# Kernel tuning notes

Measured on AMD Instinct MI355X. Metric: run time of the kernel, lower is better.

The kernel has to match this reference:

```python
import jax, jax.numpy as jnp
import numpy as np

H_SIZE = 1024
N_HEADS = 16
HEAD_DIM = H_SIZE // N_HEADS
TAU2 = 1.0
LN_EPS = 1e-5


def setup_inputs() -> dict:
    key = jax.random.key(0)
    ks = jax.random.split(key, 12)
    B, S = 2, 1024
    s = 1.0 / np.sqrt(H_SIZE)
    inp = {
        "input": jax.random.normal(ks[0], (B, S, H_SIZE), dtype=jnp.float32),
        "input_mask": jnp.ones((B, S), dtype=jnp.float32),
        # uniform(0,1) noise; converted to Gumbel(0,1) inside reference
        "gumbel": jax.random.uniform(ks[1], (B, N_HEADS, S, S), dtype=jnp.float32,
                                     minval=1e-10, maxval=1.0),
        "Wq": jax.random.normal(ks[2], (H_SIZE, H_SIZE), dtype=jnp.float32) * s,
        "bq": jnp.zeros((H_SIZE,), dtype=jnp.float32),
        "Wk": jax.random.normal(ks[3], (H_SIZE, H_SIZE), dtype=jnp.float32) * s,
        "bk": jnp.zeros((H_SIZE,), dtype=jnp.float32),
        "Wv": jax.random.normal(ks[4], (H_SIZE, H_SIZE), dtype=jnp.float32) * s,
        "bv": jnp.zeros((H_SIZE,), dtype=jnp.float32),
        "Wo": jax.random.normal(ks[5], (H_SIZE, H_SIZE), dtype=jnp.float32) * s,
        "bo": jnp.zeros((H_SIZE,), dtype=jnp.float32),
        "gamma": jnp.ones((H_SIZE,), dtype=jnp.float32),
        "beta": jnp.zeros((H_SIZE,), dtype=jnp.float32),
    }
    return inp


def reference(input, input_mask, gumbel, Wq, bq, Wk, bk, Wv, bv, Wo, bo, gamma, beta):
    B, S, _ = input.shape
    # projections -> [B, H, S, D]
    def proj(W, b):
        y = jnp.einsum('bsh,oh->bso', input, W) + b  # torch Linear: x @ W.T + b
        return y.reshape(B, S, N_HEADS, HEAD_DIM).transpose(0, 2, 1, 3)
    qq = proj(Wq, bq)
    kk = proj(Wk, bk)
    vv = proj(Wv, bv)
    # raw scores (NOTE: original has no 1/sqrt(d) scaling)
    interact = jnp.einsum('bhqd,bhkd->bhqk', qq, kk)
    # gumbel-softmax (soft): softmax((logits + g)/tau)
    g = -jnp.log(-jnp.log(gumbel))
    sto_attn = jax.nn.softmax((interact + g) / TAU2, axis=-1)
    # masking: mask_1 over query dim, mask_2 over key dim
    mask = input_mask[:, None, :, None] * input_mask[:, None, None, :]  # [B,1,S,S]
    attn = sto_attn * mask
    # (dropout p=0 -> identity)
    out = jnp.einsum('bhqk,bhkd->bhqd', attn, vv)
    out = out.transpose(0, 2, 1, 3).reshape(B, S, H_SIZE)
    out = jnp.einsum('bsh,oh->bso', out, Wo) + bo
    # residual + layernorm
    x = out + input
    mu = jnp.mean(x, axis=-1, keepdims=True)
    var = jnp.mean(jnp.square(x - mu), axis=-1, keepdims=True)
    return (x - mu) * jax.lax.rsqrt(var + LN_EPS) * gamma + beta
```

## Files before the change

kernel.cpp:

```cpp
#include <hip/hip_runtime.h>

#define S_LEN 1024
#define HSZ   1024
#define NHEAD 16
#define HD    64
#define BATCH 2
#define MROWS 2048
#define SOFTMAX_M0 50.0f

typedef unsigned short u16;
typedef __attribute__((ext_vector_type(8))) short short8;
typedef __attribute__((ext_vector_type(4))) short short4v;
typedef __attribute__((ext_vector_type(4))) float f32x4;

#define MFMA_BF16(a, b, c) __builtin_amdgcn_mfma_f32_16x16x32_bf16((a), (b), (c), 0, 0, 0)

__device__ __forceinline__ u16 f2bf(float f) {
    union { float f; unsigned u; } c; c.f = f;
    unsigned u = c.u;
    u += 0x7fffu + ((u >> 16) & 1u);
    return (u16)(u >> 16);
}
__device__ __forceinline__ float bf2f(u16 s) {
    union { unsigned u; float f; } c; c.u = ((unsigned)s) << 16;
    return c.f;
}
__device__ __forceinline__ short8 ld8(const u16* p) {
    return *reinterpret_cast<const short8*>(p);
}
__device__ __forceinline__ void gld16(const u16* g, u16* l) {
    __builtin_amdgcn_global_load_lds(
        (const __attribute__((address_space(1))) unsigned int*)g,
        (__attribute__((address_space(3))) unsigned int*)l, 16, 0, 0);
}
__device__ __forceinline__ f32x4 ld4_nt(const float* p) {
    return __builtin_nontemporal_load(reinterpret_cast<const f32x4*>(p));
}
__device__ __forceinline__ int frag_off(int row, int cbb) {
    return (((row << 3) | (cbb ^ (row & 7))) << 3);
}

template<int MT>
__device__ __forceinline__ void gemm_tile(const u16* __restrict__ Ag,
                                          const u16* __restrict__ Bg,
                                          int klen, u16* As, u16* Bs,
                                          f32x4 (&acc)[MT][4]) {
    const int tid  = threadIdx.x;
    const int wave = tid >> 6, lane = tid & 63;
    const int lr = lane & 15, grp = lane >> 4;
    const int wm = wave >> 1, wn = wave & 1;
    const int ASZ = MT * 2048;
    const int BSZ = 8192;

#pragma unroll
    for (int mt = 0; mt < MT; mt++)
#pragma unroll
        for (int nt = 0; nt < 4; nt++)
            acc[mt][nt] = (f32x4){0.f, 0.f, 0.f, 0.f};

    auto stage = [&](int k0, u16* Ah, u16* Bh) {
#pragma unroll
        for (int j = 0; j < MT; j++) {
            int c = j * 256 + tid, row = c >> 3, cb = (c & 7) ^ (row & 7);
            gld16(Ag + (size_t)row * HSZ + k0 + cb * 8, Ah + c * 8);
        }
#pragma unroll
        for (int j = 0; j < 4; j++) {
            int c = j * 256 + tid, row = c >> 3, cb = (c & 7) ^ (row & 7);
            gld16(Bg + (size_t)row * HSZ + k0 + cb * 8, Bh + c * 8);
        }
    };

    stage(0, As, Bs);

    for (int k0 = 0; k0 < klen; k0 += 64) {
        const int cur = (k0 >> 6) & 1;
        const u16* Ac = As + cur * ASZ;
        const u16* Bc = Bs + cur * BSZ;
        __syncthreads();
        if (k0 + 64 < klen)
            stage(k0 + 64, As + (cur ^ 1) * ASZ, Bs + (cur ^ 1) * BSZ);

#pragma unroll
        for (int h = 0; h < 2; h++) {
            const int cbb = h * 4 + grp;
            short8 af[MT], bf[4];
#pragma unroll
            for (int mt = 0; mt < MT; mt++)
                af[mt] = ld8(Ac + frag_off(wm * (MT * 16) + mt * 16 + lr, cbb));
#pragma unroll
            for (int nt = 0; nt < 4; nt++)
                bf[nt] = ld8(Bc + frag_off(wn * 64 + nt * 16 + lr, cbb));
#pragma unroll
            for (int mt = 0; mt < MT; mt++)
#pragma unroll
                for (int nt = 0; nt < 4; nt++)
                    acc[mt][nt] = MFMA_BF16(af[mt], bf[nt], acc[mt][nt]);
        }
    }
}

__global__ __launch_bounds__(256)
void convert_kernel(const float* __restrict__ x,  const float* __restrict__ wq,
                    const float* __restrict__ wk, const float* __restrict__ wv,
                    const float* __restrict__ wo, u16* __restrict__ dst) {
    const int XV = (MROWS * HSZ) / 4;
    const int WV = (HSZ * HSZ) / 4;
    int vid = blockIdx.x * 256 + threadIdx.x;
    const float* src; int off;
    if (vid < XV)            { src = x;  off = vid; }
    else if (vid < XV + WV)  { src = wq; off = vid - XV; }
    else if (vid < XV + 2*WV){ src = wk; off = vid - XV - WV; }
    else if (vid < XV + 3*WV){ src = wv; off = vid - XV - 2*WV; }
    else                     { src = wo; off = vid - XV - 3*WV; }
    float4 v = reinterpret_cast<const float4*>(src)[off];
    ushort4 o;
    o.x = f2bf(v.x); o.y = f2bf(v.y); o.z = f2bf(v.z); o.w = f2bf(v.w);
    reinterpret_cast<ushort4*>(dst)[vid] = o;
}

__global__ __launch_bounds__(256)
void qkv_gemm(const u16* __restrict__ xb,
              const u16* __restrict__ wqb, const u16* __restrict__ wkb,
              const u16* __restrict__ wvb,
              const float* __restrict__ bq, const float* __restrict__ bk,
              const float* __restrict__ bv, const float* __restrict__ mask,
              u16* __restrict__ qout, u16* __restrict__ kout,
              u16* __restrict__ vtout) {
    __shared__ u16 As[2 * 64 * 64];
    __shared__ u16 Bs[2 * 128 * 64];
    const int ntile = blockIdx.x;
    const int mtile = blockIdx.y;
    const int p  = ntile >> 3;
    const int m0 = mtile * 64;
    const int nw = (ntile & 7) * 128;
    const u16*  W    = (p == 0) ? wqb : (p == 1) ? wkb : wvb;
    const float* bias = (p == 0) ? bq : (p == 1) ? bk : bv;

    f32x4 acc[2][4];
    gemm_tile<2>(xb + (size_t)m0 * HSZ, W + (size_t)nw * HSZ, HSZ, As, Bs, acc);

    const int wave = threadIdx.x >> 6, lane = threadIdx.x & 63;
    const int lr = lane & 15, grp = lane >> 4;
    const int wm = wave >> 1, wn = wave & 1;
#pragma unroll
    for (int mt = 0; mt < 2; mt++)
#pragma unroll
        for (int nt = 0; nt < 4; nt++)
#pragma unroll
            for (int r = 0; r < 4; r++) {
                int m = m0 + wm * 32 + mt * 16 + grp * 4 + r;
                int o = nw + wn * 64 + nt * 16 + lr;
                float val = acc[mt][nt][r] + bias[o];
                int b = m >> 10, s = m & 1023, hh = o >> 6, d = o & 63;
                if (p == 0)
                    qout[(((size_t)(b * NHEAD + hh)) * S_LEN + s) * HD + d] = f2bf(val);
                else if (p == 1)
                    kout[(((size_t)(b * NHEAD + hh)) * S_LEN + s) * HD + d] = f2bf(val);
                else
                    vtout[(((size_t)(b * NHEAD + hh)) * HD + d) * S_LEN + s] =
                        f2bf(val * mask[m]);
            }
}

__global__ __launch_bounds__(256, 4)
void attn_kernel(const u16* __restrict__ qb, const u16* __restrict__ kb,
                 const u16* __restrict__ vt, const float* __restrict__ gumbel,
                 u16* __restrict__ po, float* __restrict__ pl) {
    const int bh   = blockIdx.y;
    const int qt   = blockIdx.x;
    const int half = blockIdx.z;
    const int q0 = qt * 64, kbase = half * 512;
    const int tid = threadIdx.x;
    const int wave = tid >> 6, lane = tid & 63;
    const int lr = lane & 15, grp = lane >> 4;

    const u16* Q = qb + (size_t)bh * S_LEN * HD;
    const u16* K = kb + (size_t)bh * S_LEN * HD;
    const u16* V = vt + (size_t)bh * HD * S_LEN;
    const int qw = q0 + wave * 16;
    const float* Gp = gumbel + (size_t)bh * S_LEN * S_LEN + (size_t)(qw + lr) * S_LEN;

    __shared__ u16 Ks[2][64 * 64];
    __shared__ u16 Vs[2][64 * 64];
    __shared__ u16 pbuf[4 * 16 * 64];
    u16* pw = pbuf + wave * (16 * 64);

    short8 aq0 = ld8(Q + (size_t)(qw + lr) * HD + grp * 8);
    short8 aq1 = ld8(Q + (size_t)(qw + lr) * HD + 32 + grp * 8);

    f32x4 acco[4];
#pragma unroll
    for (int i = 0; i < 4; i++) acco[i] = (f32x4){0.f, 0.f, 0.f, 0.f};
    float lsum = 0.f;

    f32x4 gc[4], gn[4];
#pragma unroll
    for (int kt = 0; kt < 4; kt++)
        gc[kt] = ld4_nt(Gp + kbase + kt * 16 + grp * 4);

    auto stageKV = [&](int k0, int buf) {
#pragma unroll
        for (int j = 0; j < 2; j++) {
            int c = j * 256 + tid, row = c >> 3, cb = (c & 7) ^ (row & 7);
            gld16(K + (size_t)(k0 + row) * HD + cb * 8, Ks[buf] + c * 8);
        }
#pragma unroll
        for (int j = 0; j < 2; j++) {
            int c = j * 256 + tid, row = c >> 3, cb = (c & 7) ^ (row & 7);
            gld16(V + (size_t)row * S_LEN + k0 + cb * 8, Vs[buf] + c * 8);
        }
    };
    stageKV(kbase, 0);

#pragma unroll 1
    for (int it = 0; it < 8; it++) {
        const int k0 = kbase + it * 64;
        const int cur = it & 1;

        __syncthreads();
        if (it < 7) {
            stageKV(k0 + 64, cur ^ 1);
#pragma unroll
            for (int kt = 0; kt < 4; kt++)
                gn[kt] = ld4_nt(Gp + k0 + 64 + kt * 16 + grp * 4);
        }

#pragma unroll
        for (int kt = 0; kt < 4; kt++) {
            short8 kf0 = ld8(Ks[cur] + frag_off(kt * 16 + lr, grp));
            short8 kf1 = ld8(Ks[cur] + frag_off(kt * 16 + lr, 4 + grp));
            f32x4 a = (f32x4){0.f, 0.f, 0.f, 0.f};
            a = MFMA_BF16(kf0, aq0, a);
            a = MFMA_BF16(kf1, aq1, a);
            float p[4];
#pragma unroll
            for (int r = 0; r < 4; r++) {
                float w = -__builtin_amdgcn_rcpf(__logf(gc[kt][r]));
                p[r] = __expf(a[r] - SOFTMAX_M0) * w;
                lsum += p[r];
            }
            ushort4 pk;
            pk.x = f2bf(p[0]); pk.y = f2bf(p[1]);
            pk.z = f2bf(p[2]); pk.w = f2bf(p[3]);
            *reinterpret_cast<ushort4*>(
                pw + lr * 64 + (((kt * 16 + grp * 4) ^ ((lr & 7) << 3)))) = pk;
        }

        short8 pa[2];
#pragma unroll
        for (int ks = 0; ks < 2; ks++) {
            const u16* pp = pw + lr * 64 + (((ks * 32 + grp * 8) ^ ((lr & 7) << 3)));
            short4v lo = *reinterpret_cast<const short4v*>(pp);
            short4v hi = *reinterpret_cast<const short4v*>(pp + 4);
            pa[ks] = __builtin_shufflevector(lo, hi, 0, 1, 2, 3, 4, 5, 6, 7);
        }

#pragma unroll
        for (int nt = 0; nt < 4; nt++)
#pragma unroll
            for (int ks = 0; ks < 2; ks++)
                acco[nt] = MFMA_BF16(pa[ks],
                                     ld8(Vs[cur] + frag_off(nt * 16 + lr, ks * 4 + grp)),
                                     acco[nt]);

        if (it < 7) {
#pragma unroll
            for (int kt = 0; kt < 4; kt++) gc[kt] = gn[kt];
        }
    }

    lsum += __shfl_xor(lsum, 16, 64);
    lsum += __shfl_xor(lsum, 32, 64);

    const int qbase = ((half * 32 + bh) * 16 + qt) * 64 + wave * 16;
    if (lane < 16) pl[qbase + lane] = lsum;

    const int qidx = qbase + grp * 4;
#pragma unroll
    for (int nt = 0; nt < 4; nt++)
#pragma unroll
        for (int r = 0; r < 4; r++)
            po[(size_t)(qidx + r) * 64 + nt * 16 + lr] = f2bf(acco[nt][r]);
}

__global__ __launch_bounds__(256)
void combine_kernel(const u16* __restrict__ po, const float* __restrict__ pl,
                    const float* __restrict__ mask, u16* __restrict__ ctx) {
    const int qt = blockIdx.x, bh = blockIdx.y;
    const int b = bh >> 4, h = bh & 15;
    const int q = threadIdx.x >> 2;
    const int dc = (threadIdx.x & 3) * 16;
    const int i0 = ((0 * 32 + bh) * 16 + qt) * 64 + q;
    const int i1 = ((1 * 32 + bh) * 16 + qt) * 64 + q;
    float l = pl[i0] + pl[i1];
    float mq = mask[b * S_LEN + qt * 64 + q] / l;
    u16* dst = ctx + ((size_t)(b * S_LEN + qt * 64 + q)) * HSZ + h * 64 + dc;
#pragma unroll
    for (int c = 0; c < 2; c++) {
        short8 a = ld8(po + (size_t)i0 * 64 + dc + c * 8);
        short8 bm = ld8(po + (size_t)i1 * 64 + dc + c * 8);
        short8 o;
#pragma unroll
        for (int j = 0; j < 8; j++)
            o[j] = (short)f2bf((bf2f((u16)a[j]) + bf2f((u16)bm[j])) * mq);
        *reinterpret_cast<short8*>(dst + c * 8) = o;
    }
}

__global__ __launch_bounds__(256)
void oproj_gemm(const u16* __restrict__ A, const u16* __restrict__ W,
                float* __restrict__ part0, float* __restrict__ part1) {
    __shared__ u16 As[2 * 64 * 64];
    __shared__ u16 Bs[2 * 128 * 64];
    const int ntile = blockIdx.x;
    const int mtile = blockIdx.y;
    const int z     = blockIdx.z;
    const int m0 = mtile * 64, n0 = ntile * 128, koff = z * 512;

    f32x4 acc[2][4];
    gemm_tile<2>(A + (size_t)m0 * HSZ + koff, W + (size_t)n0 * HSZ + koff,
                 512, As, Bs, acc);

    float* dst = z ? part1 : part0;
    const int wave = threadIdx.x >> 6, lane = threadIdx.x & 63;
    const int lr = lane & 15, grp = lane >> 4;
    const int wm = wave >> 1, wn = wave & 1;
#pragma unroll
    for (int mt = 0; mt < 2; mt++)
#pragma unroll
        for (int nt = 0; nt < 4; nt++)
#pragma unroll
            for (int r = 0; r < 4; r++) {
                int m = m0 + wm * 32 + mt * 16 + grp * 4 + r;
                int o = n0 + wn * 64 + nt * 16 + lr;
                dst[(size_t)m * HSZ + o] = acc[mt][nt][r];
            }
}

__global__ __launch_bounds__(256)
void ln_kernel(const float* __restrict__ part0, const float* __restrict__ part1,
               const float* __restrict__ xin, const float* __restrict__ bo,
               const float* __restrict__ gamma, const float* __restrict__ beta,
               float* __restrict__ out) {
    const int row = blockIdx.x;
    const int tid = threadIdx.x;
    const size_t base = (size_t)row * (HSZ / 4);

    float4 p0 = reinterpret_cast<const float4*>(part0)[base + tid];
    float4 p1 = reinterpret_cast<const float4*>(part1)[base + tid];
    float4 xr = reinterpret_cast<const float4*>(xin)[base + tid];
    float4 bb = reinterpret_cast<const float4*>(bo)[tid];
    float4 v;
    v.x = p0.x + p1.x + xr.x + bb.x;
    v.y = p0.y + p1.y + xr.y + bb.y;
    v.z = p0.z + p1.z + xr.z + bb.z;
    v.w = p0.w + p1.w + xr.w + bb.w;

    float s  = v.x + v.y + v.z + v.w;
    float ss = v.x * v.x + v.y * v.y + v.z * v.z + v.w * v.w;
#pragma unroll
    for (int off = 1; off < 64; off <<= 1) {
        s  += __shfl_xor(s, off, 64);
        ss += __shfl_xor(ss, off, 64);
    }
    __shared__ float red[8];
    int wave = tid >> 6, lane = tid & 63;
    if (lane == 0) { red[wave] = s; red[4 + wave] = ss; }
    __syncthreads();
    s  = red[0] + red[1] + red[2] + red[3];
    ss = red[4] + red[5] + red[6] + red[7];
    float mu  = s * (1.f / HSZ);
    float var = ss * (1.f / HSZ) - mu * mu;
    float rstd = rsqrtf(var + 1e-5f);

    float4 g  = reinterpret_cast<const float4*>(gamma)[tid];
    float4 be = reinterpret_cast<const float4*>(beta)[tid];
    float4 o;
    o.x = (v.x - mu) * rstd * g.x + be.x;
    o.y = (v.y - mu) * rstd * g.y + be.y;
    o.z = (v.z - mu) * rstd * g.z + be.z;
    o.w = (v.w - mu) * rstd * g.w + be.w;
    reinterpret_cast<float4*>(out)[base + tid] = o;
}

extern "C" void kernel_launch(void* const* d_in, const int* in_sizes, int n_in,
                              void* d_out, int out_size, void* d_ws, size_t ws_size,
                              hipStream_t stream) {
    (void)in_sizes; (void)n_in; (void)out_size; (void)ws_size;
    const float* x     = (const float*)d_in[0];
    const float* mask  = (const float*)d_in[1];
    const float* gum   = (const float*)d_in[2];
    const float* Wq    = (const float*)d_in[3];
    const float* bq    = (const float*)d_in[4];
    const float* Wk    = (const float*)d_in[5];
    const float* bk    = (const float*)d_in[6];
    const float* Wv    = (const float*)d_in[7];
    const float* bv    = (const float*)d_in[8];
    const float* Wo    = (const float*)d_in[9];
    const float* bo    = (const float*)d_in[10];
    const float* gamma = (const float*)d_in[11];
    const float* beta  = (const float*)d_in[12];
    float* out = (float*)d_out;

    u16* xb  = (u16*)d_ws;
    u16* wqb = xb  + 2097152;
    u16* wkb = wqb + 1048576;
    u16* wvb = wkb + 1048576;
    u16* wob = wvb + 1048576;
    u16* qb  = wob + 1048576;
    u16* kb  = qb  + 2097152;
    u16* vt  = kb  + 2097152;
    u16* ctx = vt  + 2097152;
    float* part0 = (float*)(ctx + 2097152);
    float* pl    = (float*)((char*)part0 + 8388608);
    u16*   po    = xb;
    float* part1 = (float*)xb;

    convert_kernel<<<dim3(6144), dim3(256), 0, stream>>>(x, Wq, Wk, Wv, Wo, xb);
    qkv_gemm<<<dim3(24, 32), dim3(256), 0, stream>>>(xb, wqb, wkb, wvb,
                                                     bq, bk, bv, mask,
                                                     qb, kb, vt);
    attn_kernel<<<dim3(16, 32, 2), dim3(256), 0, stream>>>(qb, kb, vt, gum, po, pl);
    combine_kernel<<<dim3(16, 32), dim3(256), 0, stream>>>(po, pl, mask, ctx);
    oproj_gemm<<<dim3(8, 32, 2), dim3(256), 0, stream>>>(ctx, wob, part0, part1);
    ln_kernel<<<dim3(2048), dim3(256), 0, stream>>>(part0, part1, x, bo,
                                                    gamma, beta, out);
}
```

Baseline: 293.1 us.

## Split attention key range into four chunks and drop K/V double buffering

The attention kernel now splits the key dimension into four 256-key chunks instead of two 512-key halves, doubling the grid to 2048 blocks. It drops the double-buffered K/V shared tiles to cut LDS use, and raises the occupancy hint to 6 blocks per CU. Staging becomes synchronous, with two barriers per iteration, and the combine kernel now sums four partials. The partial output buffer moves to a separate workspace region. The aim is more parallelism and latency hiding on the gumbel-bandwidth-bound kernel, at the cost of exposed K/V load latency and extra partial traffic.

Result: slower. 382.2 us (+30.4%).

```diff
diff --git a/kernel.cpp b/kernel.cpp
--- a/kernel.cpp
+++ b/kernel.cpp
@@ -163,14 +163,14 @@
             }
 }
 
-__global__ __launch_bounds__(256, 4)
+__global__ __launch_bounds__(256, 6)
 void attn_kernel(const u16* __restrict__ qb, const u16* __restrict__ kb,
                  const u16* __restrict__ vt, const float* __restrict__ gumbel,
                  u16* __restrict__ po, float* __restrict__ pl) {
-    const int bh   = blockIdx.y;
-    const int qt   = blockIdx.x;
-    const int half = blockIdx.z;
-    const int q0 = qt * 64, kbase = half * 512;
+    const int bh  = blockIdx.y;
+    const int qt  = blockIdx.x;
+    const int qtr = blockIdx.z;
+    const int q0 = qt * 64, kbase = qtr * 256;
     const int tid = threadIdx.x;
     const int wave = tid >> 6, lane = tid & 63;
     const int lr = lane & 15, grp = lane >> 4;
@@ -181,8 +181,8 @@
     const int qw = q0 + wave * 16;
     const float* Gp = gumbel + (size_t)bh * S_LEN * S_LEN + (size_t)(qw + lr) * S_LEN;
 
-    __shared__ u16 Ks[2][64 * 64];
-    __shared__ u16 Vs[2][64 * 64];
+    __shared__ u16 Ks[64 * 64];
+    __shared__ u16 Vs[64 * 64];
     __shared__ u16 pbuf[4 * 16 * 64];
     u16* pw = pbuf + wave * (16 * 64);
 
@@ -199,28 +199,24 @@
     for (int kt = 0; kt < 4; kt++)
         gc[kt] = ld4_nt(Gp + kbase + kt * 16 + grp * 4);
 
-    auto stageKV = [&](int k0, int buf) {
+#pragma unroll 1
+    for (int it = 0; it < 4; it++) {
+        const int k0 = kbase + it * 64;
+
+        __syncthreads();
 #pragma unroll
         for (int j = 0; j < 2; j++) {
             int c = j * 256 + tid, row = c >> 3, cb = (c & 7) ^ (row & 7);
-            gld16(K + (size_t)(k0 + row) * HD + cb * 8, Ks[buf] + c * 8);
+            gld16(K + (size_t)(k0 + row) * HD + cb * 8, Ks + c * 8);
         }
 #pragma unroll
         for (int j = 0; j < 2; j++) {
             int c = j * 256 + tid, row = c >> 3, cb = (c & 7) ^ (row & 7);
-            gld16(V + (size_t)row * S_LEN + k0 + cb * 8, Vs[buf] + c * 8);
-        }
-    };
-    stageKV(kbase, 0);
-
-#pragma unroll 1
-    for (int it = 0; it < 8; it++) {
-        const int k0 = kbase + it * 64;
-        const int cur = it & 1;
-
+            gld16(V + (size_t)row * S_LEN + k0 + cb * 8, Vs + c * 8);
+        }
         __syncthreads();
-        if (it < 7) {
-            stageKV(k0 + 64, cur ^ 1);
+
+        if (it < 3) {
 #pragma unroll
             for (int kt = 0; kt < 4; kt++)
                 gn[kt] = ld4_nt(Gp + k0 + 64 + kt * 16 + grp * 4);
@@ -228,8 +224,8 @@
 
 #pragma unroll
         for (int kt = 0; kt < 4; kt++) {
-            short8 kf0 = ld8(Ks[cur] + frag_off(kt * 16 + lr, grp));
-            short8 kf1 = ld8(Ks[cur] + frag_off(kt * 16 + lr, 4 + grp));
+            short8 kf0 = ld8(Ks + frag_off(kt * 16 + lr, grp));
+            short8 kf1 = ld8(Ks + frag_off(kt * 16 + lr, 4 + grp));
             f32x4 a = (f32x4){0.f, 0.f, 0.f, 0.f};
             a = MFMA_BF16(kf0, aq0, a);
             a = MFMA_BF16(kf1, aq1, a);
@@ -261,10 +257,10 @@
 #pragma unroll
             for (int ks = 0; ks < 2; ks++)
                 acco[nt] = MFMA_BF16(pa[ks],
-                                     ld8(Vs[cur] + frag_off(nt * 16 + lr, ks * 4 + grp)),
+                                     ld8(Vs + frag_off(nt * 16 + lr, ks * 4 + grp)),
                                      acco[nt]);
 
-        if (it < 7) {
+        if (it < 3) {
 #pragma unroll
             for (int kt = 0; kt < 4; kt++) gc[kt] = gn[kt];
         }
@@ -273,7 +269,7 @@
     lsum += __shfl_xor(lsum, 16, 64);
     lsum += __shfl_xor(lsum, 32, 64);
 
-    const int qbase = ((half * 32 + bh) * 16 + qt) * 64 + wave * 16;
+    const int qbase = ((qtr * 32 + bh) * 16 + qt) * 64 + wave * 16;
     if (lane < 16) pl[qbase + lane] = lsum;
 
     const int qidx = qbase + grp * 4;
@@ -291,19 +287,27 @@
     const int b = bh >> 4, h = bh & 15;
     const int q = threadIdx.x >> 2;
     const int dc = (threadIdx.x & 3) * 16;
-    const int i0 = ((0 * 32 + bh) * 16 + qt) * 64 + q;
-    const int i1 = ((1 * 32 + bh) * 16 + qt) * 64 + q;
-    float l = pl[i0] + pl[i1];
+    int idx[4];
+    float l = 0.f;
+#pragma unroll
+    for (int z = 0; z < 4; z++) {
+        idx[z] = ((z * 32 + bh) * 16 + qt) * 64 + q;
+        l += pl[idx[z]];
+    }
     float mq = mask[b * S_LEN + qt * 64 + q] / l;
     u16* dst = ctx + ((size_t)(b * S_LEN + qt * 64 + q)) * HSZ + h * 64 + dc;
 #pragma unroll
     for (int c = 0; c < 2; c++) {
-        short8 a = ld8(po + (size_t)i0 * 64 + dc + c * 8);
-        short8 bm = ld8(po + (size_t)i1 * 64 + dc + c * 8);
+        float acc[8] = {0.f, 0.f, 0.f, 0.f, 0.f, 0.f, 0.f, 0.f};
+#pragma unroll
+        for (int z = 0; z < 4; z++) {
+            short8 a = ld8(po + (size_t)idx[z] * 64 + dc + c * 8);
+#pragma unroll
+            for (int j = 0; j < 8; j++) acc[j] += bf2f((u16)a[j]);
+        }
         short8 o;
 #pragma unroll
-        for (int j = 0; j < 8; j++)
-            o[j] = (short)f2bf((bf2f((u16)a[j]) + bf2f((u16)bm[j])) * mq);
+        for (int j = 0; j < 8; j++) o[j] = (short)f2bf(acc[j] * mq);
         *reinterpret_cast<short8*>(dst + c * 8) = o;
     }
 }
@@ -414,14 +418,14 @@
     u16* ctx = vt  + 2097152;
     float* part0 = (float*)(ctx + 2097152);
     float* pl    = (float*)((char*)part0 + 8388608);
-    u16*   po    = xb;
+    u16*   po    = (u16*)((char*)pl + 524288);
     float* part1 = (float*)xb;
 
     convert_kernel<<<dim3(6144), dim3(256), 0, stream>>>(x, Wq, Wk, Wv, Wo, xb);
     qkv_gemm<<<dim3(24, 32), dim3(256), 0, stream>>>(xb, wqb, wkb, wvb,
                                                      bq, bk, bv, mask,
                                                      qb, kb, vt);
-    attn_kernel<<<dim3(16, 32, 2), dim3(256), 0, stream>>>(qb, kb, vt, gum, po, pl);
+    attn_kernel<<<dim3(16, 32, 4), dim3(256), 0, stream>>>(qb, kb, vt, gum, po, pl);
     combine_kernel<<<dim3(16, 32), dim3(256), 0, stream>>>(po, pl, mask, ctx);
     oproj_gemm<<<dim3(8, 32, 2), dim3(256), 0, stream>>>(ctx, wob, part0, part1);
     ln_kernel<<<dim3(2048), dim3(256), 0, stream>>>(part0, part1, x, bo,
```
